# Kernel tuning notes

Measured on AMD Instinct MI355X. Metric: run time of the kernel, lower is better.

The kernel has to match this reference:

```python
import jax, jax.numpy as jnp
import numpy as np

RECALL_THRESHOLD = 0.3
LAMBDA_PAUC = 0.5
NUM_CLASSES = 128
LABEL_SMOOTHING = 0.1
N_SAMPLES = 131072


def setup_inputs() -> dict:
    key = jax.random.key(0)
    k1, k2 = jax.random.split(key)
    predictions = jax.random.normal(k1, (N_SAMPLES, NUM_CLASSES), dtype=jnp.float32)
    targets = jax.random.randint(k2, (N_SAMPLES,), 0, NUM_CLASSES)
    return {"predictions": predictions, "targets": targets}


def _macro_pauc(probs, targets):
    """Vectorized (over classes) partial AUC at max_fpr = 1 - recall_threshold.

    Equivalent to the per-class torch loop: descending argsort of scores,
    cumsum TP/FP, clip the ROC curve at max_fpr with linear interpolation of
    the crossing segment, trapezoidal integration, macro-average over classes
    that have at least one positive.
    """
    N, K = probs.shape
    order = jnp.argsort(-probs, axis=0)                      # [N, K] descending per class
    t_sorted = (targets[order] == jnp.arange(K)[None, :]).astype(probs.dtype)  # [N, K]
    tps = jnp.cumsum(t_sorted, axis=0)                        # [N, K]
    fps = jnp.cumsum(1.0 - t_sorted, axis=0)                  # [N, K]
    tpr = tps / jnp.maximum(tps[-1], 1.0)
    fpr = fps / jnp.maximum(fps[-1], 1.0)

    max_fpr = 1.0 - RECALL_THRESHOLD
    # Clip fpr at max_fpr; segments fully beyond the cut get delta == 0 so
    # their tpr value is irrelevant. The crossing segment's right endpoint is
    # replaced by the linearly interpolated tpr at max_fpr (matches torch's
    # slope-based interpolation with the same 1e-8 guard).
    fpr_c = jnp.minimum(fpr, max_fpr)
    slope = (tpr[1:] - tpr[:-1]) / (fpr[1:] - fpr[:-1] + 1e-8)
    tpr_interp = tpr[:-1] + slope * (max_fpr - fpr[:-1])
    tpr_next = jnp.where(fpr[1:] <= max_fpr, tpr[1:], tpr_interp)
    delta = fpr_c[1:] - fpr_c[:-1]                            # [N-1, K]
    pauc_c = jnp.sum(delta * 0.5 * (tpr_next + tpr[:-1]), axis=0)  # [K]

    valid = (tps[-1] > 0).astype(probs.dtype)                 # macro: skip empty classes
    return jnp.sum(pauc_c * valid) / jnp.maximum(jnp.sum(valid), 1.0)


def reference(predictions, targets):
    logp = jax.nn.log_softmax(predictions, axis=1)
    probs = jnp.exp(logp)
    # CrossEntropyLoss with label smoothing (mean reduction, no class weights):
    # loss_i = (1-eps) * nll_i + eps * mean_c(-log p_ic)
    nll = -jnp.take_along_axis(logp, targets[:, None], axis=1)[:, 0]
    smooth = -jnp.mean(logp, axis=1)
    ce_loss = jnp.mean((1.0 - LABEL_SMOOTHING) * nll + LABEL_SMOOTHING * smooth)

    # torch.tensor(pauc) in the original detaches pAUC from the graph.
    pauc = jax.lax.stop_gradient(_macro_pauc(probs, targets))
    pauc_loss = 1.0 - pauc ** 2
    return (1.0 - LAMBDA_PAUC) * ce_loss + LAMBDA_PAUC * pauc_loss
```

## Files before the change

### kernel.cpp

```cpp
#include <hip/hip_runtime.h>
#include <math.h>

#define N_SAMPLES 131072
#define NUM_CLASSES 128
#define NB 256
#define MAX_FPR 0.7f
#define NBLK 256
#define ROWS_PER_BLK 512
#define HWORDS (NB / 2)
#define HPITCH 129
#define PART_WORDS (NUM_CLASSES * HWORDS)

__device__ __forceinline__ int bin_of(float x, float off ) {
    int b = (int)__fmaf_rn(x, 16.0f, off);
    return min(max(b, 0), NB - 1);
}

__global__ __launch_bounds__(1024, 4) void fused_kernel(
    const float* __restrict__ pred, const int* __restrict__ tgt,
    unsigned int* __restrict__ hPos,
    unsigned int* __restrict__ part,
    float* __restrict__ ce_accum)
{
    __shared__ unsigned int h32[NUM_CLASSES * HPITCH];
    __shared__ float wsum[16];

    const int tid  = threadIdx.x;
    const int w    = tid >> 6;
    const int lane = tid & 63;
    const int j    = lane & 15;
    const int rs   = lane >> 4;

    for (int i = tid; i < NUM_CLASSES * HPITCH; i += 1024) h32[i] = 0u;
    __syncthreads();

    const int rowBase = blockIdx.x * ROWS_PER_BLK + w * 4 + rs;

    float acc_lse = 0.0f, acc_xt = 0.0f, acc_sx = 0.0f;

    const float* rp = pred + (size_t)rowBase * 128;
    float4 a0 = *(const float4*)(rp + j * 4);
    float4 a1 = *(const float4*)(rp + 64 + j * 4);
    int    tc = tgt[rowBase];

    #pragma unroll
    for (int p = 0; p < 8; p++) {
        float4 b0, b1; int tn = 0;
        if (p < 7) {
            const float* rn = pred + (size_t)(rowBase + (p + 1) * 64) * 128;
            b0 = *(const float4*)(rn + j * 4);
            b1 = *(const float4*)(rn + 64 + j * 4);
            tn = tgt[rowBase + (p + 1) * 64];
        }

        float e = __expf(a0.x) + __expf(a0.y) + __expf(a0.z) + __expf(a0.w)
                + __expf(a1.x) + __expf(a1.y) + __expf(a1.z) + __expf(a1.w);
        #pragma unroll
        for (int o = 1; o < 16; o <<= 1) e += __shfl_xor(e, o);
        const float lse = __logf(e);
        const float off = (14.0f - lse) * 16.0f;

        const float xv[8] = {a0.x, a0.y, a0.z, a0.w, a1.x, a1.y, a1.z, a1.w};
        #pragma unroll
        for (int q = 0; q < 8; q++) {
            const int c = (q < 4) ? (j * 4 + q) : (64 + j * 4 + (q - 4));
            const int b = bin_of(xv[q], off);
            atomicAdd(&h32[c * HPITCH + (b >> 1)], (b & 1) ? 65536u : 1u);
        }

        acc_sx += (xv[0] + xv[1] + xv[2] + xv[3])
                + (xv[4] + xv[5] + xv[6] + xv[7]);
        if (j == 0) acc_lse += lse;

        {
            const int t = tc;
            float xt; bool hit = false;
            if ((t >> 2) == j)                      { xt = xv[t & 3];       hit = true; }
            else if (t >= 64 && ((t - 64) >> 2) == j) { xt = xv[4 + (t & 3)]; hit = true; }
            if (hit) {
                acc_xt += xt;
                atomicAdd(&hPos[(t << 8) | bin_of(xt, off)], 1u);
            }
        }

        a0 = b0; a1 = b1; tc = tn;
    }

    float ce = acc_lse - 0.9f * acc_xt - (0.1f / 128.0f) * acc_sx;
    #pragma unroll
    for (int o = 32; o; o >>= 1) ce += __shfl_xor(ce, o);
    if (lane == 0) wsum[w] = ce;
    __syncthreads();

    if (tid == 0) {
        float s = 0.0f;
        #pragma unroll
        for (int i = 0; i < 16; i++) s += wsum[i];
        atomicAdd(ce_accum, s);
    }

    unsigned int* out = part + (size_t)blockIdx.x * PART_WORDS;
    for (int i = tid; i < PART_WORDS; i += 1024)
        out[i] = h32[(i >> 7) * HPITCH + (i & 127)];
}

__global__ __launch_bounds__(64) void pauc_reduce(
    const unsigned int* __restrict__ part,
    const unsigned int* __restrict__ hPos,
    float* __restrict__ acc)
{
    const int k    = blockIdx.x;
    const int lane = threadIdx.x;

    unsigned int a[4] = {0u, 0u, 0u, 0u};
    const unsigned int* pk = part + k * HWORDS + (126 - 2 * lane);
    #pragma unroll 4
    for (int b = 0; b < NBLK; b++) {
        const uint2 q = *(const uint2*)(pk + (size_t)b * PART_WORDS);
        a[0] += q.y >> 16;  a[1] += q.y & 0xffffu;
        a[2] += q.x >> 16;  a[3] += q.x & 0xffffu;
    }
    const uint4 pq = ((const uint4*)(hPos + (k << 8)))[63 - lane];
    const unsigned int p[4] = {pq.w, pq.z, pq.y, pq.x};

    unsigned int la = a[0] + a[1] + a[2] + a[3];
    unsigned int lp = p[0] + p[1] + p[2] + p[3];

    unsigned int ia = la, ip = lp;
    #pragma unroll
    for (int o = 1; o < 64; o <<= 1) {
        const unsigned int ta = __shfl_up(ia, o);
        const unsigned int tp = __shfl_up(ip, o);
        if (lane >= o) { ia += ta; ip += tp; }
    }
    const unsigned int P = __shfl(ip, 63);
    const unsigned int T = __shfl(ia, 63);
    const float Pm = fmaxf((float)P, 1.0f);
    const float Fm = fmaxf((float)(T - P), 1.0f);

    int cumA = (int)(ia - la), cumP = (int)(ip - lp);
    float contrib = 0.0f;
    #pragma unroll
    for (int i = 0; i < 4; i++) {
        const int f = (int)a[i] - (int)p[i];
        if (f > 0) {
            const float fpr0 = (float)(cumA - cumP) / Fm;
            if (fpr0 < MAX_FPR) {
                const float tpr0 = (float)cumP / Pm;
                const float tpr1 = (float)(cumP + (int)p[i]) / Pm;
                const float fpr1 = (float)(cumA - cumP + f) / Fm;
                if (fpr1 <= MAX_FPR) {
                    contrib += (fpr1 - fpr0) * 0.5f * (tpr0 + tpr1);
                } else {
                    const float tfrac = (MAX_FPR - fpr0) / (fpr1 - fpr0);
                    const float tprc  = tpr0 + tfrac * (tpr1 - tpr0);
                    contrib += (MAX_FPR - fpr0) * 0.5f * (tpr0 + tprc);
                }
            }
        }
        cumA += (int)a[i]; cumP += (int)p[i];
    }

    #pragma unroll
    for (int o = 32; o; o >>= 1) contrib += __shfl_xor(contrib, o);
    if (lane == 0 && P > 0u) {
        atomicAdd(&acc[1], contrib);
        atomicAdd(&acc[2], 1.0f);
    }
}

__global__ void k5_finalize(const float* __restrict__ acc, float* __restrict__ out)
{
    const float ce    = acc[0] * (1.0f / (float)N_SAMPLES);
    const float valid = fmaxf(acc[2], 1.0f);
    const float pauc  = acc[1] / valid;
    out[0] = 0.5f * ce + 0.5f * (1.0f - pauc * pauc);
}

extern "C" void kernel_launch(void* const* d_in, const int* in_sizes, int n_in,
                              void* d_out, int out_size, void* d_ws, size_t ws_size,
                              hipStream_t stream)
{
    const float* pred = (const float*)d_in[0];
    const int*   tgt  = (const int*)d_in[1];

    char* ws = (char*)d_ws;
    unsigned int* hPos = (unsigned int*)ws;
    float*        acc  = (float*)(ws + 131072);
    unsigned int* part = (unsigned int*)(ws + 262144);

    hipMemsetAsync(hPos, 0, 131072 + 16, stream);

    fused_kernel<<<NBLK, 1024, 0, stream>>>(pred, tgt, hPos, part, acc);
    pauc_reduce<<<NUM_CLASSES, 64, 0, stream>>>(part, hPos, acc);
    k5_finalize<<<1, 1, 0, stream>>>(acc, (float*)d_out);
}
```

Baseline: 124.1 us.

## Halve fused block size, widen pAUC reduction, fold finalize into last block

Blocks in the fused histogram kernel drop to 512 threads and 256 rows, so 512 blocks are launched instead of 256 and the grid fills more CUs. The pAUC reduce now uses 256 threads per class, split into two halves that sum partial histograms through shared memory. The separate finalize launch is removed; a completion counter lets the last reduce block compute the output. The trade-off is that twice as many partial histograms (512 x 64KB) must be written and read back, which adds memory traffic.

```diff
diff --git a/kernel.cpp b/kernel.cpp
--- a/kernel.cpp
+++ b/kernel.cpp
@@ -5,8 +5,8 @@
 #define NUM_CLASSES 128
 #define NB 256
 #define MAX_FPR 0.7f
-#define NBLK 256
-#define ROWS_PER_BLK 512
+#define NBLK 512
+#define ROWS_PER_BLK 256
 #define HWORDS (NB / 2)
 #define HPITCH 129
 #define PART_WORDS (NUM_CLASSES * HWORDS)
@@ -16,14 +16,14 @@
     return min(max(b, 0), NB - 1);
 }
 
-__global__ __launch_bounds__(1024, 4) void fused_kernel(
+__global__ __launch_bounds__(512, 4) void fused_kernel(
     const float* __restrict__ pred, const int* __restrict__ tgt,
     unsigned int* __restrict__ hPos,
     unsigned int* __restrict__ part,
     float* __restrict__ ce_accum)
 {
     __shared__ unsigned int h32[NUM_CLASSES * HPITCH];
-    __shared__ float wsum[16];
+    __shared__ float wsum[8];
 
     const int tid  = threadIdx.x;
     const int w    = tid >> 6;
@@ -31,7 +31,7 @@
     const int j    = lane & 15;
     const int rs   = lane >> 4;
 
-    for (int i = tid; i < NUM_CLASSES * HPITCH; i += 1024) h32[i] = 0u;
+    for (int i = tid; i < NUM_CLASSES * HPITCH; i += 512) h32[i] = 0u;
     __syncthreads();
 
     const int rowBase = blockIdx.x * ROWS_PER_BLK + w * 4 + rs;
@@ -47,10 +47,10 @@
     for (int p = 0; p < 8; p++) {
         float4 b0, b1; int tn = 0;
         if (p < 7) {
-            const float* rn = pred + (size_t)(rowBase + (p + 1) * 64) * 128;
+            const float* rn = pred + (size_t)(rowBase + (p + 1) * 32) * 128;
             b0 = *(const float4*)(rn + j * 4);
             b1 = *(const float4*)(rn + 64 + j * 4);
-            tn = tgt[rowBase + (p + 1) * 64];
+            tn = tgt[rowBase + (p + 1) * 32];
         }
 
         float e = __expf(a0.x) + __expf(a0.y) + __expf(a0.z) + __expf(a0.w)
@@ -75,7 +75,7 @@
         {
             const int t = tc;
             float xt; bool hit = false;
-            if ((t >> 2) == j)                      { xt = xv[t & 3];       hit = true; }
+            if ((t >> 2) == j)                        { xt = xv[t & 3];       hit = true; }
             else if (t >= 64 && ((t - 64) >> 2) == j) { xt = xv[4 + (t & 3)]; hit = true; }
             if (hit) {
                 acc_xt += xt;
@@ -95,86 +95,106 @@
     if (tid == 0) {
         float s = 0.0f;
         #pragma unroll
-        for (int i = 0; i < 16; i++) s += wsum[i];
+        for (int i = 0; i < 8; i++) s += wsum[i];
         atomicAdd(ce_accum, s);
     }
 
     unsigned int* out = part + (size_t)blockIdx.x * PART_WORDS;
-    for (int i = tid; i < PART_WORDS; i += 1024)
+    for (int i = tid; i < PART_WORDS; i += 512)
         out[i] = h32[(i >> 7) * HPITCH + (i & 127)];
 }
 
-__global__ __launch_bounds__(64) void pauc_reduce(
+__global__ __launch_bounds__(256) void pauc_reduce(
     const unsigned int* __restrict__ part,
     const unsigned int* __restrict__ hPos,
-    float* __restrict__ acc)
+    float* __restrict__ acc,
+    float* __restrict__ out)
 {
+    __shared__ __align__(16) unsigned int sA[NB];
+
     const int k    = blockIdx.x;
-    const int lane = threadIdx.x;
-
-    unsigned int a[4] = {0u, 0u, 0u, 0u};
-    const unsigned int* pk = part + k * HWORDS + (126 - 2 * lane);
-    #pragma unroll 4
-    for (int b = 0; b < NBLK; b++) {
-        const uint2 q = *(const uint2*)(pk + (size_t)b * PART_WORDS);
-        a[0] += q.y >> 16;  a[1] += q.y & 0xffffu;
-        a[2] += q.x >> 16;  a[3] += q.x & 0xffffu;
-    }
-    const uint4 pq = ((const uint4*)(hPos + (k << 8)))[63 - lane];
-    const unsigned int p[4] = {pq.w, pq.z, pq.y, pq.x};
-
-    unsigned int la = a[0] + a[1] + a[2] + a[3];
-    unsigned int lp = p[0] + p[1] + p[2] + p[3];
-
-    unsigned int ia = la, ip = lp;
-    #pragma unroll
-    for (int o = 1; o < 64; o <<= 1) {
-        const unsigned int ta = __shfl_up(ia, o);
-        const unsigned int tp = __shfl_up(ip, o);
-        if (lane >= o) { ia += ta; ip += tp; }
-    }
-    const unsigned int P = __shfl(ip, 63);
-    const unsigned int T = __shfl(ia, 63);
-    const float Pm = fmaxf((float)P, 1.0f);
-    const float Fm = fmaxf((float)(T - P), 1.0f);
-
-    int cumA = (int)(ia - la), cumP = (int)(ip - lp);
-    float contrib = 0.0f;
-    #pragma unroll
-    for (int i = 0; i < 4; i++) {
-        const int f = (int)a[i] - (int)p[i];
-        if (f > 0) {
-            const float fpr0 = (float)(cumA - cumP) / Fm;
-            if (fpr0 < MAX_FPR) {
-                const float tpr0 = (float)cumP / Pm;
-                const float tpr1 = (float)(cumP + (int)p[i]) / Pm;
-                const float fpr1 = (float)(cumA - cumP + f) / Fm;
-                if (fpr1 <= MAX_FPR) {
-                    contrib += (fpr1 - fpr0) * 0.5f * (tpr0 + tpr1);
-                } else {
-                    const float tfrac = (MAX_FPR - fpr0) / (fpr1 - fpr0);
-                    const float tprc  = tpr0 + tfrac * (tpr1 - tpr0);
-                    contrib += (MAX_FPR - fpr0) * 0.5f * (tpr0 + tprc);
+    const int t    = threadIdx.x;
+    const int w    = t & 127;
+    const int half = t >> 7;
+
+    unsigned int lo = 0u, hi = 0u;
+    const unsigned int* p0 = part + (size_t)(half * (NBLK / 2)) * PART_WORDS
+                                  + k * HWORDS + w;
+    #pragma unroll 8
+    for (int b = 0; b < NBLK / 2; b++) {
+        const unsigned int q = p0[(size_t)b * PART_WORDS];
+        lo += q & 0xffffu; hi += q >> 16;
+    }
+    if (half == 0) { sA[2 * w] = lo; sA[2 * w + 1] = hi; }
+    __syncthreads();
+    if (half == 1) { sA[2 * w] += lo; sA[2 * w + 1] += hi; }
+    __syncthreads();
+
+    if (t < 64) {
+        const int lane = t;
+        const uint4 q  = ((const uint4*)sA)[63 - lane];
+        const unsigned int a[4] = {q.w, q.z, q.y, q.x};
+        const uint4 pq = ((const uint4*)(hPos + (k << 8)))[63 - lane];
+        const unsigned int p[4] = {pq.w, pq.z, pq.y, pq.x};
+
+        const unsigned int la = a[0] + a[1] + a[2] + a[3];
+        const unsigned int lp = p[0] + p[1] + p[2] + p[3];
+
+        unsigned int ia = la, ip = lp;
+        #pragma unroll
+        for (int o = 1; o < 64; o <<= 1) {
+            const unsigned int ta = __shfl_up(ia, o);
+            const unsigned int tp = __shfl_up(ip, o);
+            if (lane >= o) { ia += ta; ip += tp; }
+        }
+        const unsigned int P = __shfl(ip, 63);
+        const unsigned int T = __shfl(ia, 63);
+        const float Pm = fmaxf((float)P, 1.0f);
+        const float Fm = fmaxf((float)(T - P), 1.0f);
+
+        int cumA = (int)(ia - la), cumP = (int)(ip - lp);
+        float contrib = 0.0f;
+        #pragma unroll
+        for (int i = 0; i < 4; i++) {
+            const int f = (int)a[i] - (int)p[i];
+            if (f > 0) {
+                const float fpr0 = (float)(cumA - cumP) / Fm;
+                if (fpr0 < MAX_FPR) {
+                    const float tpr0 = (float)cumP / Pm;
+                    const float tpr1 = (float)(cumP + (int)p[i]) / Pm;
+                    const float fpr1 = (float)(cumA - cumP + f) / Fm;
+                    if (fpr1 <= MAX_FPR) {
+                        contrib += (fpr1 - fpr0) * 0.5f * (tpr0 + tpr1);
+                    } else {
+                        const float tfrac = (MAX_FPR - fpr0) / (fpr1 - fpr0);
+                        const float tprc  = tpr0 + tfrac * (tpr1 - tpr0);
+                        contrib += (MAX_FPR - fpr0) * 0.5f * (tpr0 + tprc);
+                    }
                 }
             }
-        }
-        cumA += (int)a[i]; cumP += (int)p[i];
-    }
-
-    #pragma unroll
-    for (int o = 32; o; o >>= 1) contrib += __shfl_xor(contrib, o);
-    if (lane == 0 && P > 0u) {
-        atomicAdd(&acc[1], contrib);
-        atomicAdd(&acc[2], 1.0f);
-    }
-}
-
-__global__ void k5_finalize(const float* __restrict__ acc, float* __restrict__ out)
-{
-    const float ce    = acc[0] * (1.0f / (float)N_SAMPLES);
-    const float valid = fmaxf(acc[2], 1.0f);
-    const float pauc  = acc[1] / valid;
-    out[0] = 0.5f * ce + 0.5f * (1.0f - pauc * pauc);
+            cumA += (int)a[i]; cumP += (int)p[i];
+        }
+
+        #pragma unroll
+        for (int o = 32; o; o >>= 1) contrib += __shfl_xor(contrib, o);
+
+        if (lane == 0) {
+            if (P > 0u) {
+                atomicAdd(&acc[1], contrib);
+                atomicAdd(&acc[2], 1.0f);
+            }
+            __threadfence();
+            const unsigned int done = atomicAdd((unsigned int*)(acc + 3), 1u);
+            if (done == NUM_CLASSES - 1) {
+                const float ces = atomicAdd(&acc[0], 0.0f);
+                const float ps  = atomicAdd(&acc[1], 0.0f);
+                const float vs  = atomicAdd(&acc[2], 0.0f);
+                const float ce   = ces * (1.0f / (float)N_SAMPLES);
+                const float pauc = ps / fmaxf(vs, 1.0f);
+                out[0] = 0.5f * ce + 0.5f * (1.0f - pauc * pauc);
+            }
+        }
+    }
 }
 
 extern "C" void kernel_launch(void* const* d_in, const int* in_sizes, int n_in,
@@ -191,7 +211,6 @@
 
     hipMemsetAsync(hPos, 0, 131072 + 16, stream);
 
-    fused_kernel<<<NBLK, 1024, 0, stream>>>(pred, tgt, hPos, part, acc);
-    pauc_reduce<<<NUM_CLASSES, 64, 0, stream>>>(part, hPos, acc);
-    k5_finalize<<<1, 1, 0, stream>>>(acc, (float*)d_out);
-}
+    fused_kernel<<<NBLK, 512, 0, stream>>>(pred, tgt, hPos, part, acc);
+    pauc_reduce<<<NUM_CLASSES, 256, 0, stream>>>(part, hPos, acc, (float*)d_out);
+}
```

New measurement: 116.5 us. 1.07x faster.
